# Kernel optimization log

Measured on AMD Instinct MI355X. Metric: run time of the kernel, lower is better.

## Reference

```python
import jax, jax.numpy as jnp
import numpy as np

D = 4       # number of TT dimensions
N = 128     # mode size per dimension (Ns)
R = 16      # TT rank (RMAX)
B = 262144  # batch of query points


def setup_inputs() -> dict:
    key = jax.random.key(0)
    ks = jax.random.split(key, 5)
    # points in [-1, 1] (remap_needed=True assumes this domain)
    x = jax.random.uniform(ks[0], (B, D), dtype=jnp.float32) * 2.0 - 1.0
    core0 = jax.random.normal(ks[1], (1, N, R), dtype=jnp.float32)
    core1 = jax.random.normal(ks[2], (R, N, R), dtype=jnp.float32)
    core2 = jax.random.normal(ks[3], (R, N, R), dtype=jnp.float32)
    core3 = jax.random.normal(ks[4], (R, N, 1), dtype=jnp.float32)
    return {"x": x, "core0": core0, "core1": core1, "core2": core2, "core3": core3}


def _forward(x, cores):
    # remap: (x + 1) / 2 * (Ns[0] - 1)  (module uses Ns[0] for all dims)
    n0 = cores[0].shape[1]
    xr = (x + 1.0) * 0.5 * (n0 - 1)
    # per-dim clamp to [0, Ns[i]-1]
    ns = jnp.array([c.shape[1] for c in cores], dtype=x.dtype)  # [D]
    xc = jnp.clip(xr, 0.0, ns - 1.0)  # broadcast over D
    idx_low = jnp.floor(xc).astype(jnp.int32)   # [B, D]
    idx_high = jnp.ceil(xc).astype(jnp.int32)   # [B, D]
    wh = xc - idx_low.astype(x.dtype)           # [B, D] interpolation weights
    # gather + linear interpolation per core -> list of [r_prev, B, r_next]
    newcores = []
    for i, c in enumerate(cores):
        lo = jnp.take(c, idx_low[:, i], axis=1)   # [r_prev, B, r_next]
        hi = jnp.take(c, idx_high[:, i], axis=1)  # [r_prev, B, r_next]
        w = wh[:, i][None, :, None]               # [1, B, 1]
        newcores.append((1.0 - w) * lo + w * hi)
    # chained batched contraction, right to left (matches ttcontract)
    res = newcores[-1]
    for i in range(len(newcores) - 2, 0, -1):
        res = jnp.einsum('abc,cbk->abk', newcores[i], res)
    return jnp.einsum('abc,cbk->b', newcores[0], res)  # [B]


def reference(x, core0, core1, core2, core3):
    return _forward(x, [core0, core1, core2, core3])
```

## Files before the change

kernel.cpp:

```cpp
#include <hip/hip_runtime.h>
#include <hip/hip_bf16.h>

typedef unsigned int uint32;
typedef unsigned short u16;

#define NPT 128
#define RNK 16
#define ROW_U16 256
#define EDGEROW 20
#define NWAVES 16
#define SMEM_BYTES (2*NPT*ROW_U16*2 + 2*NPT*EDGEROW*4 + 2*NWAVES*64*4)

#if defined(__has_builtin)
#if __has_builtin(__builtin_amdgcn_fdot2_f32_bf16)
#define HAVE_BFDOT2 1
#endif
#endif

__device__ __forceinline__ float bl(uint32 u){ return __uint_as_float(u << 16); }
__device__ __forceinline__ float bh(uint32 u){ return __uint_as_float(u & 0xffff0000u); }

#ifdef HAVE_BFDOT2
typedef __bf16 v2bf __attribute__((ext_vector_type(2)));
__device__ __forceinline__ v2bf bc(uint32 u){ return __builtin_bit_cast(v2bf, u); }
__device__ __forceinline__ float dot8(const uint32* vp, uint4 U) {
  float s = 0.f;
  s = __builtin_amdgcn_fdot2_f32_bf16(bc(vp[0]), bc(U.x), s, false);
  s = __builtin_amdgcn_fdot2_f32_bf16(bc(vp[1]), bc(U.y), s, false);
  s = __builtin_amdgcn_fdot2_f32_bf16(bc(vp[2]), bc(U.z), s, false);
  s = __builtin_amdgcn_fdot2_f32_bf16(bc(vp[3]), bc(U.w), s, false);
  return s;
}
#else
__device__ __forceinline__ float dot8(const uint32* vp, uint4 U) {
  float s = fmaf(bh(vp[0]), bh(U.x), bl(vp[0]) * bl(U.x));
  s = fmaf(bl(vp[1]), bl(U.y), s); s = fmaf(bh(vp[1]), bh(U.y), s);
  s = fmaf(bl(vp[2]), bl(U.z), s); s = fmaf(bh(vp[2]), bh(U.z), s);
  s = fmaf(bl(vp[3]), bl(U.w), s); s = fmaf(bh(vp[3]), bh(U.w), s);
  return s;
}
#endif

__device__ __forceinline__ uint32 packbf(float a, float b) {
  __hip_bfloat16 l = __float2bfloat16(a), h = __float2bfloat16(b);
  return (uint32)(*(u16*)&l) | ((uint32)(*(u16*)&h) << 16);
}

__device__ __forceinline__ float remap_clamp(float x) {
  float xr = (x + 1.0f) * 0.5f * (float)(NPT - 1);
  return fminf(fmaxf(xr, 0.0f), (float)(NPT - 1));
}

__device__ __forceinline__ void mid_dim2(const u16* __restrict__ c, float xcA, float xcB,
                                         int q, const uint32* vpA, const uint32* vpB,
                                         float& nA0, float& nA1, float& nB0, float& nB1)
{
  int a0 = (int)xcA; float wA = xcA - (float)a0; int a1 = min(a0 + 1, NPT - 1);
  int b0 = (int)xcB; float wB = xcB - (float)b0; int b1 = min(b0 + 1, NPT - 1);
  const uint32* rA0 = (const uint32*)(c + a0 * ROW_U16) + q * 4;
  const uint32* rA1 = (const uint32*)(c + a1 * ROW_U16) + q * 4;
  const uint32* rB0 = (const uint32*)(c + b0 * ROW_U16) + q * 4;
  const uint32* rB1 = (const uint32*)(c + b1 * ROW_U16) + q * 4;
  uint4 A0 = *(const uint4*)(rA0);      uint4 A1 = *(const uint4*)(rA0 + 32);
  uint4 A2 = *(const uint4*)(rA0 + 64); uint4 A3 = *(const uint4*)(rA0 + 96);
  uint4 A4 = *(const uint4*)(rA1);      uint4 A5 = *(const uint4*)(rA1 + 32);
  uint4 A6 = *(const uint4*)(rA1 + 64); uint4 A7 = *(const uint4*)(rA1 + 96);
  uint4 B0 = *(const uint4*)(rB0);      uint4 B1 = *(const uint4*)(rB0 + 32);
  uint4 B2 = *(const uint4*)(rB0 + 64); uint4 B3 = *(const uint4*)(rB0 + 96);
  uint4 B4 = *(const uint4*)(rB1);      uint4 B5 = *(const uint4*)(rB1 + 32);
  uint4 B6 = *(const uint4*)(rB1 + 64); uint4 B7 = *(const uint4*)(rB1 + 96);
  float aA0 = dot8(vpA, A0) + dot8(vpA + 4, A1);
  float aA1 = dot8(vpA, A4) + dot8(vpA + 4, A5);
  float bA0 = dot8(vpA, A2) + dot8(vpA + 4, A3);
  float bA1 = dot8(vpA, A6) + dot8(vpA + 4, A7);
  float aB0 = dot8(vpB, B0) + dot8(vpB + 4, B1);
  float aB1 = dot8(vpB, B4) + dot8(vpB + 4, B5);
  float bB0 = dot8(vpB, B2) + dot8(vpB + 4, B3);
  float bB1 = dot8(vpB, B6) + dot8(vpB + 4, B7);
  nA0 = fmaf(wA, aA1 - aA0, aA0);
  nA1 = fmaf(wA, bA1 - bA0, bA0);
  nB0 = fmaf(wB, aB1 - aB0, aB0);
  nB1 = fmaf(wB, bB1 - bB0, bB0);
}

__device__ __forceinline__ void exchange2(uint32* xchA, uint32* xchB, int lane,
                                          float nA0, float nA1, float nB0, float nB1,
                                          uint32* vpA, uint32* vpB)
{
  xchA[lane] = packbf(nA0, nA1);
  xchB[lane] = packbf(nB0, nB1);
  __asm__ volatile("s_waitcnt lgkmcnt(0)" ::: "memory");
  const uint4* a = (const uint4*)(xchA + (lane & 56));
  const uint4* b = (const uint4*)(xchB + (lane & 56));
  uint4 a0 = a[0], a1 = a[1], b0 = b[0], b1 = b[1];
  vpA[0]=a0.x; vpA[1]=a0.y; vpA[2]=a0.z; vpA[3]=a0.w;
  vpA[4]=a1.x; vpA[5]=a1.y; vpA[6]=a1.z; vpA[7]=a1.w;
  vpB[0]=b0.x; vpB[1]=b0.y; vpB[2]=b0.z; vpB[3]=b0.w;
  vpB[4]=b1.x; vpB[5]=b1.y; vpB[6]=b1.z; vpB[7]=b1.w;
}

__global__ __launch_bounds__(1024, 4) void tt_kernel(
    const float* __restrict__ x,  const float* __restrict__ g0,
    const float* __restrict__ g1, const float* __restrict__ g2,
    const float* __restrict__ g3, float* __restrict__ out, int npts)
{
  extern __shared__ char smem[];
  u16* c1 = (u16*)smem;
  u16* c2 = c1 + NPT * ROW_U16;
  float* c0 = (float*)(c2 + NPT * ROW_U16);
  float* c3 = c0 + NPT * EDGEROW;
  uint32* xch = (uint32*)(c3 + NPT * EDGEROW);

  for (int t = threadIdx.x; t < RNK * NPT * RNK; t += blockDim.x) {
    int i = t >> 11;
    int n = (t >> 4) & (NPT - 1);
    int j = t & (RNK - 1);
    int slot = (j >> 1) + ((i >> 3) << 3) + ((j & 1) << 4);
    int off = n * ROW_U16 + slot * 8 + (i & 7);
    __hip_bfloat16 h1 = __float2bfloat16(g1[t]);
    __hip_bfloat16 h2 = __float2bfloat16(g2[t]);
    c1[off] = *(u16*)&h1;
    c2[off] = *(u16*)&h2;
  }
  for (int t = threadIdx.x; t < NPT * RNK; t += blockDim.x) {
    int n = t >> 4;
    int i = t & (RNK - 1);
    c0[n * EDGEROW + i] = g0[t];
    c3[n * EDGEROW + i] = g3[i * NPT + n];
  }
  __syncthreads();

  const int lane = threadIdx.x & 63;
  const int q = threadIdx.x & 7;
  uint32* xchA = xch + (threadIdx.x >> 6) * 128;
  uint32* xchB = xchA + 64;
  const int ptb = threadIdx.x >> 3;

  for (int it = 0; it < 4; ++it) {
    int pA = (blockIdx.x << 10) + (it << 8) + ptb;
    int pB = pA + 128;
    bool okA = pA < npts, okB = pB < npts;
    float4 xvA = reinterpret_cast<const float4*>(x)[okA ? pA : 0];
    float4 xvB = reinterpret_cast<const float4*>(x)[okB ? pB : 0];

    uint32 vpA[8], vpB[8];
    float nA0, nA1, nB0, nB1;
    {
      float xcA = remap_clamp(xvA.x);
      int n0 = (int)xcA; float w = xcA - (float)n0; int n1 = min(n0 + 1, NPT - 1);
      float2 lo = *(const float2*)(c0 + n0 * EDGEROW + 2 * q);
      float2 hi = *(const float2*)(c0 + n1 * EDGEROW + 2 * q);
      nA0 = fmaf(w, hi.x - lo.x, lo.x);
      nA1 = fmaf(w, hi.y - lo.y, lo.y);
      float xcB = remap_clamp(xvB.x);
      int m0 = (int)xcB; float u = xcB - (float)m0; int m1 = min(m0 + 1, NPT - 1);
      float2 lo2 = *(const float2*)(c0 + m0 * EDGEROW + 2 * q);
      float2 hi2 = *(const float2*)(c0 + m1 * EDGEROW + 2 * q);
      nB0 = fmaf(u, hi2.x - lo2.x, lo2.x);
      nB1 = fmaf(u, hi2.y - lo2.y, lo2.y);
    }
    exchange2(xchA, xchB, lane, nA0, nA1, nB0, nB1, vpA, vpB);
    mid_dim2(c1, remap_clamp(xvA.y), remap_clamp(xvB.y), q, vpA, vpB, nA0, nA1, nB0, nB1);
    exchange2(xchA, xchB, lane, nA0, nA1, nB0, nB1, vpA, vpB);
    mid_dim2(c2, remap_clamp(xvA.z), remap_clamp(xvB.z), q, vpA, vpB, nA0, nA1, nB0, nB1);
    {
      float xcA = remap_clamp(xvA.w);
      int n0 = (int)xcA; float w = xcA - (float)n0; int n1 = min(n0 + 1, NPT - 1);
      float2 lo = *(const float2*)(c3 + n0 * EDGEROW + 2 * q);
      float2 hi = *(const float2*)(c3 + n1 * EDGEROW + 2 * q);
      float xcB = remap_clamp(xvB.w);
      int m0 = (int)xcB; float u = xcB - (float)m0; int m1 = min(m0 + 1, NPT - 1);
      float2 lo2 = *(const float2*)(c3 + m0 * EDGEROW + 2 * q);
      float2 hi2 = *(const float2*)(c3 + m1 * EDGEROW + 2 * q);
      float pa = fmaf(nA1, fmaf(w, hi.y - lo.y, lo.y), nA0 * fmaf(w, hi.x - lo.x, lo.x));
      float pb = fmaf(nB1, fmaf(u, hi2.y - lo2.y, lo2.y), nB0 * fmaf(u, hi2.x - lo2.x, lo2.x));
      pa += __shfl_xor(pa, 1, 64);  pb += __shfl_xor(pb, 1, 64);
      pa += __shfl_xor(pa, 2, 64);  pb += __shfl_xor(pb, 2, 64);
      pa += __shfl_xor(pa, 4, 64);  pb += __shfl_xor(pb, 4, 64);
      if (q == 0) {
        if (okA) out[pA] = pa;
        if (okB) out[pB] = pb;
      }
    }
  }
}

extern "C" void kernel_launch(void* const* d_in, const int* in_sizes, int n_in,
                              void* d_out, int out_size, void* d_ws, size_t ws_size,
                              hipStream_t stream) {
  const float* x  = (const float*)d_in[0];
  const float* g0 = (const float*)d_in[1];
  const float* g1 = (const float*)d_in[2];
  const float* g2 = (const float*)d_in[3];
  const float* g3 = (const float*)d_in[4];
  float* out = (float*)d_out;

  int B = in_sizes[0] / 4;
  hipFuncSetAttribute(reinterpret_cast<const void*>(tt_kernel),
                      hipFuncAttributeMaxDynamicSharedMemorySize, SMEM_BYTES);
  int block = 1024;
  int grid = (B + 1024 - 1) / 1024;
  tt_kernel<<<grid, block, SMEM_BYTES, stream>>>(x, g0, g1, g2, g3, out, B);
}
```

Measured before the change: 83.81 us.

## Split TT kernel into two stages with prepacked bf16 cores

```diff
diff --git a/kernel.cpp b/kernel.cpp
--- a/kernel.cpp
+++ b/kernel.cpp
@@ -7,9 +7,13 @@
 #define NPT 128
 #define RNK 16
 #define ROW_U16 256
+#define ROW_U32 128
 #define EDGEROW 20
+#define CORE_U32 (NPT*ROW_U32)
+#define CORE_BYTES (CORE_U32*4)
+#define SMEM_AB (CORE_BYTES + NPT*EDGEROW*4)
 #define NWAVES 16
-#define SMEM_BYTES (2*NPT*ROW_U16*2 + 2*NPT*EDGEROW*4 + 2*NWAVES*64*4)
+#define SMEM_FB (2*NPT*ROW_U16*2 + 2*NPT*EDGEROW*4 + 2*NWAVES*64*4)
 
 #if defined(__has_builtin)
 #if __has_builtin(__builtin_amdgcn_fdot2_f32_bf16)
@@ -49,6 +53,141 @@
 __device__ __forceinline__ float remap_clamp(float x) {
   float xr = (x + 1.0f) * 0.5f * (float)(NPT - 1);
   return fminf(fmaxf(xr, 0.0f), (float)(NPT - 1));
+}
+
+__device__ __forceinline__ void allgather8(int q, uint32 m, uint32* vp) {
+  uint32 o1 = (uint32)__shfl_xor((int)m, 1, 64);
+  uint32 a0 = (q & 1) ? o1 : m;
+  uint32 a1 = (q & 1) ? m : o1;
+  uint32 b0 = (uint32)__shfl_xor((int)a0, 2, 64);
+  uint32 b1 = (uint32)__shfl_xor((int)a1, 2, 64);
+  uint32 c0 = (q & 2) ? b0 : a0;
+  uint32 c1 = (q & 2) ? b1 : a1;
+  uint32 c2 = (q & 2) ? a0 : b0;
+  uint32 c3 = (q & 2) ? a1 : b1;
+  uint32 d0 = (uint32)__shfl_xor((int)c0, 4, 64);
+  uint32 d1 = (uint32)__shfl_xor((int)c1, 4, 64);
+  uint32 d2 = (uint32)__shfl_xor((int)c2, 4, 64);
+  uint32 d3 = (uint32)__shfl_xor((int)c3, 4, 64);
+  if (q & 4) { vp[0]=d0; vp[1]=d1; vp[2]=d2; vp[3]=d3; vp[4]=c0; vp[5]=c1; vp[6]=c2; vp[7]=c3; }
+  else       { vp[0]=c0; vp[1]=c1; vp[2]=c2; vp[3]=c3; vp[4]=d0; vp[5]=d1; vp[6]=d2; vp[7]=d3; }
+}
+
+__device__ __forceinline__ void mid_dim(const u16* __restrict__ c, float xc, int q,
+                                        const uint32* vp, float& nv0, float& nv1)
+{
+  int n0 = (int)xc;
+  float w = xc - (float)n0;
+  int n1 = min(n0 + 1, NPT - 1);
+  const uint32* r0 = (const uint32*)(c + n0 * ROW_U16) + q * 4;
+  const uint32* r1 = (const uint32*)(c + n1 * ROW_U16) + q * 4;
+  uint4 A0 = *(const uint4*)(r0);
+  uint4 A1 = *(const uint4*)(r0 + 32);
+  uint4 A2 = *(const uint4*)(r0 + 64);
+  uint4 A3 = *(const uint4*)(r0 + 96);
+  uint4 B0 = *(const uint4*)(r1);
+  uint4 B1 = *(const uint4*)(r1 + 32);
+  uint4 B2 = *(const uint4*)(r1 + 64);
+  uint4 B3 = *(const uint4*)(r1 + 96);
+  float a0 = dot8(vp, A0) + dot8(vp + 4, A1);
+  float a1 = dot8(vp, B0) + dot8(vp + 4, B1);
+  float b0 = dot8(vp, A2) + dot8(vp + 4, A3);
+  float b1 = dot8(vp, B2) + dot8(vp + 4, B3);
+  nv0 = fmaf(w, a1 - a0, a0);
+  nv1 = fmaf(w, b1 - b0, b0);
+}
+
+__global__ void prep_cores(const float* __restrict__ g1, const float* __restrict__ g2,
+                           uint32* __restrict__ ws) {
+  int t = blockIdx.x * blockDim.x + threadIdx.x;
+  const float* g = (t < CORE_U32) ? g1 : g2;
+  int o = t & (CORE_U32 - 1);
+  int n = o >> 7;
+  int k = o & 127;
+  int s = k >> 2;
+  int ip = k & 3;
+  int j = ((s & 7) << 1) | (s >> 4);
+  int i = ((s >> 3) & 1) * 8 + ip * 2;
+  float lo = g[i * 2048 + n * 16 + j];
+  float hi = g[(i + 1) * 2048 + n * 16 + j];
+  ws[t] = packbf(lo, hi);
+}
+
+__global__ __launch_bounds__(1024, 8) void ttA(
+    const float* __restrict__ x, const float* __restrict__ g0,
+    const uint32* __restrict__ wsc, uint32* __restrict__ vbuf, int npts)
+{
+  extern __shared__ char smem[];
+  u16* c1 = (u16*)smem;
+  float* c0 = (float*)(smem + CORE_BYTES);
+
+  {
+    const uint4* src = (const uint4*)wsc;
+    uint4* dst = (uint4*)c1;
+    for (int t = threadIdx.x; t < CORE_U32 / 4; t += blockDim.x) dst[t] = src[t];
+  }
+  for (int t = threadIdx.x; t < NPT * RNK; t += blockDim.x)
+    c0[(t >> 4) * EDGEROW + (t & 15)] = g0[t];
+  __syncthreads();
+
+  const int q = threadIdx.x & 7;
+  const int ptb = threadIdx.x >> 3;
+  for (int it = 0; it < 4; ++it) {
+    int p = (blockIdx.x << 9) + (it << 7) + ptb;
+    int pc = min(p, npts - 1);
+    float2 xy = *(const float2*)(x + pc * 4);
+    float xc = remap_clamp(xy.x);
+    int n0 = (int)xc; float w = xc - (float)n0; int n1 = min(n0 + 1, NPT - 1);
+    float2 lo = *(const float2*)(c0 + n0 * EDGEROW + 2 * q);
+    float2 hi = *(const float2*)(c0 + n1 * EDGEROW + 2 * q);
+    float nv0 = fmaf(w, hi.x - lo.x, lo.x);
+    float nv1 = fmaf(w, hi.y - lo.y, lo.y);
+    uint32 vp[8];
+    allgather8(q, packbf(nv0, nv1), vp);
+    mid_dim(c1, remap_clamp(xy.y), q, vp, nv0, nv1);
+    if (p < npts) vbuf[p * 8 + q] = packbf(nv0, nv1);
+  }
+}
+
+__global__ __launch_bounds__(1024, 8) void ttB(
+    const float* __restrict__ x, const float* __restrict__ g3,
+    const uint32* __restrict__ wsc, const uint32* __restrict__ vbuf,
+    float* __restrict__ out, int npts)
+{
+  extern __shared__ char smem[];
+  u16* c2 = (u16*)smem;
+  float* c3 = (float*)(smem + CORE_BYTES);
+
+  {
+    const uint4* src = (const uint4*)(wsc + CORE_U32);
+    uint4* dst = (uint4*)c2;
+    for (int t = threadIdx.x; t < CORE_U32 / 4; t += blockDim.x) dst[t] = src[t];
+  }
+  for (int t = threadIdx.x; t < NPT * RNK; t += blockDim.x)
+    c3[(t & 127) * EDGEROW + (t >> 7)] = g3[t];
+  __syncthreads();
+
+  const int q = threadIdx.x & 7;
+  const int ptb = threadIdx.x >> 3;
+  for (int it = 0; it < 4; ++it) {
+    int p = (blockIdx.x << 9) + (it << 7) + ptb;
+    int pc = min(p, npts - 1);
+    float2 zw = *(const float2*)(x + pc * 4 + 2);
+    uint32 m = vbuf[pc * 8 + q];
+    uint32 vp[8];
+    allgather8(q, m, vp);
+    float nv0, nv1;
+    mid_dim(c2, remap_clamp(zw.x), q, vp, nv0, nv1);
+    float xc = remap_clamp(zw.y);
+    int n0 = (int)xc; float w = xc - (float)n0; int n1 = min(n0 + 1, NPT - 1);
+    float2 lo = *(const float2*)(c3 + n0 * EDGEROW + 2 * q);
+    float2 hi = *(const float2*)(c3 + n1 * EDGEROW + 2 * q);
+    float part = fmaf(nv1, fmaf(w, hi.y - lo.y, lo.y), nv0 * fmaf(w, hi.x - lo.x, lo.x));
+    part += __shfl_xor(part, 1, 64);
+    part += __shfl_xor(part, 2, 64);
+    part += __shfl_xor(part, 4, 64);
+    if (q == 0 && p < npts) out[p] = part;
+  }
 }
 
 __device__ __forceinline__ void mid_dim2(const u16* __restrict__ c, float xcA, float xcB,
@@ -99,7 +238,7 @@
   vpB[4]=b1.x; vpB[5]=b1.y; vpB[6]=b1.z; vpB[7]=b1.w;
 }
 
-__global__ __launch_bounds__(1024, 4) void tt_kernel(
+__global__ __launch_bounds__(1024, 4) void tt_fb(
     const float* __restrict__ x,  const float* __restrict__ g0,
     const float* __restrict__ g1, const float* __restrict__ g2,
     const float* __restrict__ g3, float* __restrict__ out, int npts)
@@ -142,7 +281,6 @@
     bool okA = pA < npts, okB = pB < npts;
     float4 xvA = reinterpret_cast<const float4*>(x)[okA ? pA : 0];
     float4 xvB = reinterpret_cast<const float4*>(x)[okB ? pB : 0];
-
     uint32 vpA[8], vpB[8];
     float nA0, nA1, nB0, nB1;
     {
@@ -196,9 +334,23 @@
   float* out = (float*)d_out;
 
   int B = in_sizes[0] / 4;
-  hipFuncSetAttribute(reinterpret_cast<const void*>(tt_kernel),
-                      hipFuncAttributeMaxDynamicSharedMemorySize, SMEM_BYTES);
-  int block = 1024;
-  int grid = (B + 1024 - 1) / 1024;
-  tt_kernel<<<grid, block, SMEM_BYTES, stream>>>(x, g0, g1, g2, g3, out, B);
-}
+  size_t ws_need = (size_t)2 * CORE_BYTES + (size_t)B * 32;
+
+  if (ws_size >= ws_need) {
+    uint32* ws = (uint32*)d_ws;
+    uint32* vbuf = ws + 2 * CORE_U32;
+    hipFuncSetAttribute(reinterpret_cast<const void*>(ttA),
+                        hipFuncAttributeMaxDynamicSharedMemorySize, SMEM_AB);
+    hipFuncSetAttribute(reinterpret_cast<const void*>(ttB),
+                        hipFuncAttributeMaxDynamicSharedMemorySize, SMEM_AB);
+    prep_cores<<<128, 256, 0, stream>>>(g1, g2, ws);
+    int grid = (B + 511) / 512;
+    ttA<<<grid, 1024, SMEM_AB, stream>>>(x, g0, ws, vbuf, B);
+    ttB<<<grid, 1024, SMEM_AB, stream>>>(x, g3, ws, vbuf, out, B);
+  } else {
+    hipFuncSetAttribute(reinterpret_cast<const void*>(tt_fb),
+                        hipFuncAttributeMaxDynamicSharedMemorySize, SMEM_FB);
+    int grid = (B + 1023) / 1024;
+    tt_fb<<<grid, 1024, SMEM_FB, stream>>>(x, g0, g1, g2, g3, out, B);
+  }
+}
```

Result: slower. 86.47 us (+3.2%).
